# Kernel optimization log

Hardware: AMD Instinct MI355X
Metric: run time of the kernel (lower is better)

Reference implementation:

```python
import jax, jax.numpy as jnp
import numpy as np

NUM_CLASS = 20
ALPHA = 1.0
BETA = 1.0
IGNORE = 255


def _fdiff(f, ax):
    """np.gradient/torch.gradient with unit spacing along axis ax (edge_order=1)."""
    n = f.shape[ax]
    sl = lambda a, b: jax.lax.slice_in_dim(f, a, b, axis=ax)
    interior = (sl(2, n) - sl(0, n - 2)) * 0.5
    first = sl(1, 2) - sl(0, 1)
    last = sl(n - 1, n) - sl(n - 2, n - 1)
    return jnp.concatenate([first, interior, last], axis=ax)


def _lga(targets):
    # one-hot over all classes at once: [C, B, D, H, W]
    cls = jnp.arange(NUM_CLASS, dtype=targets.dtype)[:, None, None, None, None]
    oh = (targets[None] == cls).astype(jnp.float32)
    res = jnp.zeros(targets.shape, jnp.float32)
    for ax in (2, 3, 4):  # spatial dims of [C,B,D,H,W]
        res = res + jnp.sum(jnp.abs(_fdiff(oh, ax)), axis=0)
    return res  # [B, D, H, W]


def setup_inputs() -> dict:
    key = jax.random.key(0)
    k1, k2, k3, k4 = jax.random.split(key, 4)
    B, D, H, W = 1, 256, 256, 32
    predictions = jax.random.normal(k1, (B, NUM_CLASS, D, H, W), dtype=jnp.float32)
    targets = jax.random.randint(k2, (B, D, H, W), 0, NUM_CLASS)
    ignore = jax.random.uniform(k3, (B, D, H, W)) < 0.02
    targets = jnp.where(ignore, IGNORE, targets).astype(jnp.int32)
    class_weights = jax.random.uniform(k4, (NUM_CLASS,), dtype=jnp.float32) + 0.1
    return {"predictions": predictions, "targets": targets, "class_weights": class_weights}


def reference(predictions, targets, class_weights):
    targets = targets.astype(jnp.int32)
    valid = targets != IGNORE
    t = jnp.where(valid, targets, 0)
    # weighted CE, reduction='none': -w[t] * log_softmax(pred)[t], 0 at ignore
    logp = jax.nn.log_softmax(predictions, axis=1)
    logp_t = jnp.take_along_axis(logp, t[:, None], axis=1)[:, 0]  # [B,D,H,W]
    w = class_weights[t]
    loss = jnp.where(valid, -w * logp_t, 0.0)
    lga_weights = ALPHA + BETA * _lga(targets)
    num = jnp.sum(loss * lga_weights)
    den = jnp.sum(jnp.where(valid, w, 0.0))
    return num / den
```

## Files before the change

### kernel.cpp

```cpp
#include <hip/hip_runtime.h>

#define NUM_CLASS 20
#define IGNORE_V 255
#define WW 32
#define HH 256
#define DDEPTH 256
#define NVOX (DDEPTH * HH * WW)
#define CHUNK 1024
#define NBLK (NVOX / CHUNK)

#define WAITVM(N)  asm volatile("s_waitcnt vmcnt(" #N ")" ::: "memory")
#define WAITLGKM0  asm volatile("s_waitcnt lgkmcnt(0)" ::: "memory")

__device__ __forceinline__ float fpair(int a, int b) {
    return (a == b) ? 0.0f : ((a == IGNORE_V || b == IGNORE_V) ? 1.0f : 2.0f);
}

__device__ __forceinline__ void stage16(const float* gsrc, float* ldst) {
    __builtin_amdgcn_global_load_lds(
        (const __attribute__((address_space(1))) void*)gsrc,
        (__attribute__((address_space(3))) void*)ldst,
        16, 0, 0);
}

__global__ __launch_bounds__(256) void pal_main(
    const float* __restrict__ pred,
    const int*   __restrict__ tgt,
    const float* __restrict__ cw,
    float2*      __restrict__ partial)
{
    __shared__ __align__(16) float lbuf[4][2][5][256];
    __shared__ float lcw[NUM_CLASS];
    if (threadIdx.x < NUM_CLASS) lcw[threadIdx.x] = cw[threadIdx.x];
    __syncthreads();

    const int tid  = threadIdx.x;
    const int lane = tid & 63;
    const int wid  = tid >> 6;
    const int base = blockIdx.x * CHUNK;
    const int v0   = base + tid * 4;
    const int w0   = v0 & (WW - 1);
    const int h    = (v0 >> 5) & (HH - 1);
    const int d    = v0 >> 13;

    const int4 t4  = *reinterpret_cast<const int4*>(tgt + v0);
    const int tm1  = tgt[v0 - ((w0 != 0) ? 1 : 0)];
    const int tp4  = tgt[v0 + 3 + ((w0 != WW - 4) ? 1 : 0)];
    const int4 tu4 = *reinterpret_cast<const int4*>(tgt + v0 - ((h != 0)          ? WW      : 0));
    const int4 td4 = *reinterpret_cast<const int4*>(tgt + v0 + ((h != HH - 1)     ? WW      : 0));
    const int4 tb4 = *reinterpret_cast<const int4*>(tgt + v0 - ((d != 0)          ? WW * HH : 0));
    const int4 tf4 = *reinterpret_cast<const int4*>(tgt + v0 + ((d != DDEPTH - 1) ? WW * HH : 0));

    const int t[4] = {t4.x, t4.y, t4.z, t4.w};
    const float* gw = pred + base + wid * 256 + lane * 4;

    float s[4]  = {0.f, 0.f, 0.f, 0.f};
    float pt[4] = {0.f, 0.f, 0.f, 0.f};

    auto consume = [&](int b, int c0) {
        #pragma unroll
        for (int k = 0; k < 5; k++) {
            const float4 x = *reinterpret_cast<const float4*>(&lbuf[wid][b][k][lane * 4]);
            const int c = c0 + k;
            const float xx[4] = {x.x, x.y, x.z, x.w};
            #pragma unroll
            for (int j = 0; j < 4; j++) {
                s[j] += __expf(xx[j]);
                if (t[j] == c) pt[j] = xx[j];
            }
        }
        WAITLGKM0;
    };

    #pragma unroll
    for (int k = 0; k < 5; k++) stage16(gw + (size_t)k        * NVOX, &lbuf[wid][0][k][0]);
    #pragma unroll
    for (int k = 0; k < 5; k++) stage16(gw + (size_t)(5 + k)  * NVOX, &lbuf[wid][1][k][0]);
    WAITVM(5);  consume(0, 0);
    #pragma unroll
    for (int k = 0; k < 5; k++) stage16(gw + (size_t)(10 + k) * NVOX, &lbuf[wid][0][k][0]);
    WAITVM(5);  consume(1, 5);
    #pragma unroll
    for (int k = 0; k < 5; k++) stage16(gw + (size_t)(15 + k) * NVOX, &lbuf[wid][1][k][0]);
    WAITVM(5);  consume(0, 10);
    WAITVM(0);  consume(1, 15);

    const int tu[4] = {tu4.x, tu4.y, tu4.z, tu4.w};
    const int td[4] = {td4.x, td4.y, td4.z, td4.w};
    const int tb[4] = {tb4.x, tb4.y, tb4.z, tb4.w};
    const int tf[4] = {tf4.x, tf4.y, tf4.z, tf4.w};
    const float scH = (h == 0 || h == HH - 1)     ? 1.0f : 0.5f;
    const float scD = (d == 0 || d == DDEPTH - 1) ? 1.0f : 0.5f;

    float num = 0.0f, den = 0.0f;
    #pragma unroll
    for (int j = 0; j < 4; j++) {
        const int tj = t[j];
        if (tj != IGNORE_V) {
            const int wj = w0 + j;
            const int tL = (j > 0) ? t[j-1] : ((w0 == 0)      ? t[0] : tm1);
            const int tR = (j < 3) ? t[j+1] : ((w0 == WW - 4) ? t[3] : tp4);
            const float scW = (wj == 0 || wj == WW - 1) ? 1.0f : 0.5f;
            const float lga = scW * fpair(tL, tR)
                            + scH * fpair(tu[j], td[j])
                            + scD * fpair(tb[j], tf[j]);
            const float wt = lcw[tj];
            num += wt * (__logf(s[j]) - pt[j]) * (1.0f + lga);
            den += wt;
        }
    }

    #pragma unroll
    for (int off = 32; off > 0; off >>= 1) {
        num += __shfl_down(num, off);
        den += __shfl_down(den, off);
    }
    __shared__ float sn[4], sd[4];
    if (lane == 0) { sn[wid] = num; sd[wid] = den; }
    __syncthreads();
    if (tid == 0)
        partial[blockIdx.x] = make_float2((sn[0] + sn[1]) + (sn[2] + sn[3]),
                                          (sd[0] + sd[1]) + (sd[2] + sd[3]));
}

__global__ __launch_bounds__(256) void pal_final(
    const float2* __restrict__ partial, float* __restrict__ out)
{
    const float4* p4 = reinterpret_cast<const float4*>(partial);
    float num = 0.f, den = 0.f;
    #pragma unroll
    for (int k = 0; k < 4; k++) {
        const float4 f = p4[threadIdx.x + 256 * k];
        num += f.x + f.z;
        den += f.y + f.w;
    }
    #pragma unroll
    for (int off = 32; off > 0; off >>= 1) {
        num += __shfl_down(num, off);
        den += __shfl_down(den, off);
    }
    __shared__ float sn[4], sd[4];
    const int lane = threadIdx.x & 63;
    const int wid  = threadIdx.x >> 6;
    if (lane == 0) { sn[wid] = num; sd[wid] = den; }
    __syncthreads();
    if (threadIdx.x == 0)
        out[0] = ((sn[0] + sn[1]) + (sn[2] + sn[3])) /
                 ((sd[0] + sd[1]) + (sd[2] + sd[3]));
}

extern "C" void kernel_launch(void* const* d_in, const int* in_sizes, int n_in,
                              void* d_out, int out_size, void* d_ws, size_t ws_size,
                              hipStream_t stream) {
    const float* pred = (const float*)d_in[0];
    const int*   tgt  = (const int*)d_in[1];
    const float* cw   = (const float*)d_in[2];
    float*  out     = (float*)d_out;
    float2* partial = (float2*)d_ws;

    pal_main<<<NBLK, 256, 0, stream>>>(pred, tgt, cw, partial);
    pal_final<<<1, 256, 0, stream>>>(partial, out);
}
```

Baseline: 247.7 us.

## Split class loads between LDS DMA staging and direct register loads

The four-stage double-buffered LDS pipeline, which relied on hand-placed vmcnt/lgkmcnt waits, is replaced by two phases. In each phase, five classes are staged into a shared block-wide LDS buffer with global_load_lds while another five classes are loaded directly into registers as float4. The idea is to overlap the two load paths and halve LDS usage, which may allow more resident blocks per CU. The cost is block-wide __syncthreads barriers, plus reliance on the compiler to insert the waits that ensure the LDS DMA has completed before the buffer is read.

After: 245.6 us. About the same (-0.8%).

```diff
diff --git a/kernel.cpp b/kernel.cpp
--- a/kernel.cpp
+++ b/kernel.cpp
@@ -8,9 +8,6 @@
 #define NVOX (DDEPTH * HH * WW)
 #define CHUNK 1024
 #define NBLK (NVOX / CHUNK)
-
-#define WAITVM(N)  asm volatile("s_waitcnt vmcnt(" #N ")" ::: "memory")
-#define WAITLGKM0  asm volatile("s_waitcnt lgkmcnt(0)" ::: "memory")
 
 __device__ __forceinline__ float fpair(int a, int b) {
     return (a == b) ? 0.0f : ((a == IGNORE_V || b == IGNORE_V) ? 1.0f : 2.0f);
@@ -29,10 +26,9 @@
     const float* __restrict__ cw,
     float2*      __restrict__ partial)
 {
-    __shared__ __align__(16) float lbuf[4][2][5][256];
+    __shared__ __align__(16) float lbuf[5][CHUNK];
     __shared__ float lcw[NUM_CLASS];
     if (threadIdx.x < NUM_CLASS) lcw[threadIdx.x] = cw[threadIdx.x];
-    __syncthreads();
 
     const int tid  = threadIdx.x;
     const int lane = tid & 63;
@@ -50,40 +46,55 @@
     const int4 td4 = *reinterpret_cast<const int4*>(tgt + v0 + ((h != HH - 1)     ? WW      : 0));
     const int4 tb4 = *reinterpret_cast<const int4*>(tgt + v0 - ((d != 0)          ? WW * HH : 0));
     const int4 tf4 = *reinterpret_cast<const int4*>(tgt + v0 + ((d != DDEPTH - 1) ? WW * HH : 0));
+    const int t[4] = {t4.x, t4.y, t4.z, t4.w};
 
-    const int t[4] = {t4.x, t4.y, t4.z, t4.w};
     const float* gw = pred + base + wid * 256 + lane * 4;
+    const float* gt = pred + v0;
 
     float s[4]  = {0.f, 0.f, 0.f, 0.f};
     float pt[4] = {0.f, 0.f, 0.f, 0.f};
 
-    auto consume = [&](int b, int c0) {
+    __syncthreads();
+
+    #pragma unroll
+    for (int ph = 0; ph < 2; ph++) {
+        const int cD = ph * 10;
+        const int cV = ph * 10 + 5;
+
+        #pragma unroll
+        for (int k = 0; k < 5; k++)
+            stage16(gw + (size_t)(cD + k) * NVOX, &lbuf[k][wid * 256]);
+        float4 x[5];
+        #pragma unroll
+        for (int k = 0; k < 5; k++)
+            x[k] = *reinterpret_cast<const float4*>(gt + (size_t)(cV + k) * NVOX);
+
         #pragma unroll
         for (int k = 0; k < 5; k++) {
-            const float4 x = *reinterpret_cast<const float4*>(&lbuf[wid][b][k][lane * 4]);
-            const int c = c0 + k;
-            const float xx[4] = {x.x, x.y, x.z, x.w};
+            const int c = cV + k;
+            const float xx[4] = {x[k].x, x[k].y, x[k].z, x[k].w};
             #pragma unroll
             for (int j = 0; j < 4; j++) {
                 s[j] += __expf(xx[j]);
                 if (t[j] == c) pt[j] = xx[j];
             }
         }
-        WAITLGKM0;
-    };
 
-    #pragma unroll
-    for (int k = 0; k < 5; k++) stage16(gw + (size_t)k        * NVOX, &lbuf[wid][0][k][0]);
-    #pragma unroll
-    for (int k = 0; k < 5; k++) stage16(gw + (size_t)(5 + k)  * NVOX, &lbuf[wid][1][k][0]);
-    WAITVM(5);  consume(0, 0);
-    #pragma unroll
-    for (int k = 0; k < 5; k++) stage16(gw + (size_t)(10 + k) * NVOX, &lbuf[wid][0][k][0]);
-    WAITVM(5);  consume(1, 5);
-    #pragma unroll
-    for (int k = 0; k < 5; k++) stage16(gw + (size_t)(15 + k) * NVOX, &lbuf[wid][1][k][0]);
-    WAITVM(5);  consume(0, 10);
-    WAITVM(0);  consume(1, 15);
+        __syncthreads();
+
+        #pragma unroll
+        for (int k = 0; k < 5; k++) {
+            const float4 x2 = *reinterpret_cast<const float4*>(&lbuf[k][tid * 4]);
+            const int c = cD + k;
+            const float xx[4] = {x2.x, x2.y, x2.z, x2.w};
+            #pragma unroll
+            for (int j = 0; j < 4; j++) {
+                s[j] += __expf(xx[j]);
+                if (t[j] == c) pt[j] = xx[j];
+            }
+        }
+        __syncthreads();
+    }
 
     const int tu[4] = {tu4.x, tu4.y, tu4.z, tu4.w};
     const int td[4] = {td4.x, td4.y, td4.z, td4.w};
```
